# Performance work log

Measured on AMD Instinct MI355X. Metric: run time of the kernel, lower is better.

Reference implementation:

```python
import jax, jax.numpy as jnp
import numpy as np

B, N, D = 1024, 8192, 128
BETA = 0.25


def setup_inputs() -> dict:
    key = jax.random.key(0)
    kx, kw = jax.random.split(key)
    x = jax.random.normal(kx, (B, D), dtype=jnp.float32)
    # nn.Embedding weight init: uniform(-1/num_embeddings, 1/num_embeddings)
    W = jax.random.uniform(kw, (N, D), dtype=jnp.float32, minval=-1.0 / N, maxval=1.0 / N)
    return {"x": x, "W": W}


def reference(x, W):
    # Squared L2 distances: (B, N) via expansion; single GEMM for the cross term.
    dist = (x * x).sum(axis=1, keepdims=True) - 2.0 * (x @ W.T) + (W * W).sum(axis=1)[None, :]
    # (-dist).topk(k=1) == argmin(dist); torch keeps the k dim -> ind is (B, 1)
    ind = jnp.argmin(dist, axis=1)[:, None]
    q = W[ind]  # (B, 1, D) codebook gather (matches torch embedding(ind) shape)
    # Faithful to source: (B, D) broadcasts against (B, 1, D) -> (B, B, D)
    loss = BETA * jnp.mean((x - jax.lax.stop_gradient(q)) ** 2) + jnp.mean((jax.lax.stop_gradient(x) - q) ** 2)
    quantized = x + jax.lax.stop_gradient(q - x)  # straight-through; (B, B, D) per source broadcast
    return quantized, ind, loss
```

## Files before the change

kernel.cpp:

```cpp
#include <hip/hip_runtime.h>
#include <stdint.h>

typedef float vfloat4 __attribute__((ext_vector_type(4)));

static const long long QN       = 134217728LL;
static const long long IND_OFF  = QN;
static const long long LOSS_OFF = QN + 1024;
static const long long PVAL_OFF = 1022LL * 131072 + 128;
static const long long PIDX_OFF = 1023LL * 131072 + 128;

#define WS_W2  0
#define WS_X2  8192
#define WS_SX  9216
#define WS_SQ  9344
#define WS_SX2 9472
#define WS_SQ2 9473

__global__ void k_zero(float* __restrict__ ws) {
    int i = blockIdx.x * 256 + threadIdx.x;
    if (i < 258) ws[WS_SX + i] = 0.0f;
}

__global__ void k_rowsq(const float* __restrict__ P, float* __restrict__ o) {
    int n = blockIdx.x * 256 + threadIdx.x;
    const float4* pr = (const float4*)P + (size_t)n * 32;
    float s = 0.0f;
#pragma unroll 8
    for (int t = 0; t < 32; ++t) {
        float4 v = pr[t];
        s += v.x * v.x + v.y * v.y + v.z * v.z + v.w * v.w;
    }
    o[n] = s;
}

__global__ void k_colsums(const float* __restrict__ p, long long rowStride,
                          float* __restrict__ scol, float* __restrict__ s2out) {
    __shared__ float sh[256];
    const int tid = threadIdx.x;
    const int d = tid & 127, g = tid >> 7;
    const int r0 = blockIdx.x * 128;
    float sum = 0.0f, s2 = 0.0f;
    for (int r = r0 + g; r < r0 + 128; r += 2) {
        float v = p[(size_t)r * rowStride + d];
        sum += v;
        s2 += v * v;
    }
    sh[tid] = sum;
    __syncthreads();
    if (tid < 128) atomicAdd(&scol[d], sh[tid] + sh[tid + 128]);
    __syncthreads();
    sh[tid] = s2;
    __syncthreads();
    for (int s = 128; s > 0; s >>= 1) {
        if (tid < s) sh[tid] += sh[tid + s];
        __syncthreads();
    }
    if (tid == 0) atomicAdd(s2out, sh[0]);
}

__global__ __launch_bounds__(256) void k_score(
    const float* __restrict__ x, const float* __restrict__ W,
    const float* __restrict__ w2, const float* __restrict__ x2,
    float* __restrict__ pval, int* __restrict__ pidx) {
    __shared__ float Xs[32][132];
    __shared__ float Wst[32][132];
    const int tid = threadIdx.x;
    const int tx = tid & 15, ty = tid >> 4;
    const int n0 = blockIdx.x * 128, m0 = blockIdx.y * 128;
    const float4* xv = (const float4*)x;
    const float4* wv = (const float4*)W;

    float acc[8][8];
#pragma unroll
    for (int i = 0; i < 8; ++i)
#pragma unroll
        for (int j = 0; j < 8; ++j) acc[i][j] = 0.0f;

    for (int kc = 0; kc < 4; ++kc) {
#pragma unroll
        for (int it = 0; it < 4; ++it) {
            int f = it * 256 + tid;
            int m = f >> 3, kq = f & 7;
            float4 a = xv[(size_t)(m0 + m) * 32 + kc * 8 + kq];
            float4 b = wv[(size_t)(n0 + m) * 32 + kc * 8 + kq];
            Xs[kq * 4 + 0][m] = a.x;
            Xs[kq * 4 + 1][m] = a.y;
            Xs[kq * 4 + 2][m] = a.z;
            Xs[kq * 4 + 3][m] = a.w;
            Wst[kq * 4 + 0][m] = b.x;
            Wst[kq * 4 + 1][m] = b.y;
            Wst[kq * 4 + 2][m] = b.z;
            Wst[kq * 4 + 3][m] = b.w;
        }
        __syncthreads();
#pragma unroll 8
        for (int k = 0; k < 32; ++k) {
            float4 a0 = *(const float4*)&Xs[k][ty * 8];
            float4 a1 = *(const float4*)&Xs[k][ty * 8 + 4];
            float4 b0 = *(const float4*)&Wst[k][tx * 8];
            float4 b1 = *(const float4*)&Wst[k][tx * 8 + 4];
            float af[8] = {a0.x, a0.y, a0.z, a0.w, a1.x, a1.y, a1.z, a1.w};
            float bf[8] = {b0.x, b0.y, b0.z, b0.w, b1.x, b1.y, b1.z, b1.w};
#pragma unroll
            for (int i = 0; i < 8; ++i)
#pragma unroll
                for (int j = 0; j < 8; ++j) acc[i][j] += af[i] * bf[j];
        }
        __syncthreads();
    }

    float w2v[8];
#pragma unroll
    for (int j = 0; j < 8; ++j) w2v[j] = w2[n0 + tx * 8 + j];

#pragma unroll
    for (int i = 0; i < 8; ++i) {
        const int row = m0 + ty * 8 + i;
        const float xxv = x2[row];
        float bestv;
        int besti = n0 + tx * 8;
        {
            float t = xxv - 2.0f * acc[i][0];
            bestv = t + w2v[0];
        }
#pragma unroll
        for (int j = 1; j < 8; ++j) {
            float t = xxv - 2.0f * acc[i][j];
            float s = t + w2v[j];
            if (s < bestv) { bestv = s; besti = n0 + tx * 8 + j; }
        }
        for (int off = 1; off < 16; off <<= 1) {
            float ov = __shfl_xor(bestv, off, 64);
            int oi = __shfl_xor(besti, off, 64);
            if (ov < bestv || (ov == bestv && oi < besti)) { bestv = ov; besti = oi; }
        }
        if (tx == 0) {
            pval[row * 64 + blockIdx.x] = bestv;
            pidx[row * 64 + blockIdx.x] = besti;
        }
    }
}

__global__ void k_argmin(const float* __restrict__ W, const float* __restrict__ pval,
                         const int* __restrict__ pidx, float* __restrict__ out) {
    int r = blockIdx.x * 256 + threadIdx.x;
    float bestv = pval[r * 64];
    int besti = pidx[r * 64];
    for (int c = 1; c < 64; ++c) {
        float v = pval[r * 64 + c];
        if (v < bestv) { bestv = v; besti = pidx[r * 64 + c]; }
    }
    out[IND_OFF + r] = (float)besti;
    float4* q = (float4*)out + (size_t)r * 32768;
    const float4* wr = (const float4*)W + (size_t)besti * 32;
#pragma unroll 8
    for (int t = 0; t < 32; ++t) q[t] = wr[t];
}

__global__ void k_loss(const float* __restrict__ ws, float* __restrict__ out) {
    __shared__ float sh[128];
    int tid = threadIdx.x;
    sh[tid] = ws[WS_SX + tid] * ws[WS_SQ + tid];
    __syncthreads();
    for (int s = 64; s > 0; s >>= 1) {
        if (tid < s) sh[tid] += sh[tid + s];
        __syncthreads();
    }
    if (tid == 0) {
        double dot = (double)sh[0];
        double Sx2 = (double)ws[WS_SX2], Sq2 = (double)ws[WS_SQ2];
        double loss = 1.25 * (1024.0 * Sx2 + 1024.0 * Sq2 - 2.0 * dot) / 134217728.0;
        out[LOSS_OFF] = (float)loss;
    }
}

__global__ __launch_bounds__(256) void k_bcast(float* __restrict__ out) {
    const int i = blockIdx.x;
    const int t = threadIdx.x & 31;
    const int j0 = threadIdx.x >> 5;
    const vfloat4* src = (const vfloat4*)out + (size_t)i * 32768;
    vfloat4 q = src[t];
    vfloat4* dst = (vfloat4*)out + (size_t)i * 32768 + t;
    for (int j = j0; j < 1024; j += 8) {
        __builtin_nontemporal_store(q, dst + (size_t)j * 32);
    }
}

extern "C" void kernel_launch(void* const* d_in, const int* in_sizes, int n_in,
                              void* d_out, int out_size, void* d_ws, size_t ws_size,
                              hipStream_t stream) {
    const float* x = (const float*)d_in[0];
    const float* W = (const float*)d_in[1];
    float* out = (float*)d_out;
    float* ws = (float*)d_ws;

    hipLaunchKernelGGL(k_zero, dim3(2), dim3(256), 0, stream, ws);
    hipLaunchKernelGGL(k_rowsq, dim3(32), dim3(256), 0, stream, W, ws + WS_W2);
    hipLaunchKernelGGL(k_rowsq, dim3(4), dim3(256), 0, stream, x, ws + WS_X2);
    hipLaunchKernelGGL(k_colsums, dim3(8), dim3(256), 0, stream, x, (long long)128,
                       ws + WS_SX, ws + WS_SX2);
    hipLaunchKernelGGL(k_score, dim3(64, 8), dim3(256), 0, stream, x, W,
                       ws + WS_W2, ws + WS_X2, out + PVAL_OFF, (int*)(out + PIDX_OFF));
    hipLaunchKernelGGL(k_argmin, dim3(4), dim3(256), 0, stream, W, out + PVAL_OFF,
                       (const int*)(out + PIDX_OFF), out);
    hipLaunchKernelGGL(k_colsums, dim3(8), dim3(256), 0, stream, out, (long long)131072,
                       ws + WS_SQ, ws + WS_SQ2);
    hipLaunchKernelGGL(k_loss, dim3(1), dim3(128), 0, stream, ws, out);
    hipLaunchKernelGGL(k_bcast, dim3(1024), dim3(256), 0, stream, out);
}
```

Measured before the change: 640.9 us.

## Fuse prep, loss and broadcast kernels; split broadcast grid and drop nontemporal stores

Merges zeroing, row-norm and column-sum work into one prep kernel. The q column sums and the sum of q squared move into the argmin kernel through wave shuffles and atomics, and the loss reduction moves into block 0 of the broadcast kernel. Together this cuts the launch count from nine to four. The broadcast grid grows from 1024 to 4096 blocks, each writing a quarter of one slab, and the stores become ordinary rather than nontemporal, which may change write-back behaviour on the 512MB output. Loss is computed while other broadcast blocks are overwriting the output, but it reads only workspace, and the pval/pidx scratch that lives inside the output is consumed before the broadcast starts.

Result: no change. 635.9 us (-0.8%).

```diff
diff --git a/kernel.cpp b/kernel.cpp
--- a/kernel.cpp
+++ b/kernel.cpp
@@ -13,49 +13,39 @@
 #define WS_X2  8192
 #define WS_SX  9216
 #define WS_SQ  9344
-#define WS_SX2 9472
-#define WS_SQ2 9473
-
-__global__ void k_zero(float* __restrict__ ws) {
-    int i = blockIdx.x * 256 + threadIdx.x;
-    if (i < 258) ws[WS_SX + i] = 0.0f;
-}
-
-__global__ void k_rowsq(const float* __restrict__ P, float* __restrict__ o) {
-    int n = blockIdx.x * 256 + threadIdx.x;
-    const float4* pr = (const float4*)P + (size_t)n * 32;
-    float s = 0.0f;
+#define WS_SQ2 9472
+
+__global__ __launch_bounds__(256) void k_prep(const float* __restrict__ x,
+                                              const float* __restrict__ W,
+                                              float* __restrict__ ws) {
+    const int b = blockIdx.x, tid = threadIdx.x;
+    if (b < 36) {
+        const float4* pr = (b < 32) ? ((const float4*)W + (size_t)(b * 256 + tid) * 32)
+                                    : ((const float4*)x + (size_t)((b - 32) * 256 + tid) * 32);
+        float s = 0.0f;
 #pragma unroll 8
-    for (int t = 0; t < 32; ++t) {
-        float4 v = pr[t];
-        s += v.x * v.x + v.y * v.y + v.z * v.z + v.w * v.w;
-    }
-    o[n] = s;
-}
-
-__global__ void k_colsums(const float* __restrict__ p, long long rowStride,
-                          float* __restrict__ scol, float* __restrict__ s2out) {
-    __shared__ float sh[256];
-    const int tid = threadIdx.x;
-    const int d = tid & 127, g = tid >> 7;
-    const int r0 = blockIdx.x * 128;
-    float sum = 0.0f, s2 = 0.0f;
-    for (int r = r0 + g; r < r0 + 128; r += 2) {
-        float v = p[(size_t)r * rowStride + d];
-        sum += v;
-        s2 += v * v;
-    }
-    sh[tid] = sum;
-    __syncthreads();
-    if (tid < 128) atomicAdd(&scol[d], sh[tid] + sh[tid + 128]);
-    __syncthreads();
-    sh[tid] = s2;
-    __syncthreads();
-    for (int s = 128; s > 0; s >>= 1) {
-        if (tid < s) sh[tid] += sh[tid + s];
-        __syncthreads();
-    }
-    if (tid == 0) atomicAdd(s2out, sh[0]);
+        for (int t = 0; t < 32; ++t) {
+            float4 v = pr[t];
+            s += v.x * v.x + v.y * v.y + v.z * v.z + v.w * v.w;
+        }
+        if (b < 32) ws[WS_W2 + b * 256 + tid] = s;
+        else        ws[WS_X2 + (b - 32) * 256 + tid] = s;
+    } else {
+        __shared__ float sh[8][32];
+        const int c = tid & 31, g = tid >> 5;
+        const int col = (b - 36) * 32 + c;
+        float sum = 0.0f;
+        for (int r = g; r < 1024; r += 8) sum += x[(size_t)r * 128 + col];
+        sh[g][c] = sum;
+        __syncthreads();
+        if (g == 0) {
+            float t = 0.0f;
+#pragma unroll
+            for (int gg = 0; gg < 8; ++gg) t += sh[gg][c];
+            ws[WS_SX + col] = t;
+        }
+        if (b == 36 && tid < 129) ws[WS_SQ + tid] = 0.0f;
+    }
 }
 
 __global__ __launch_bounds__(256) void k_score(
@@ -141,9 +131,11 @@
     }
 }
 
-__global__ void k_argmin(const float* __restrict__ W, const float* __restrict__ pval,
-                         const int* __restrict__ pidx, float* __restrict__ out) {
-    int r = blockIdx.x * 256 + threadIdx.x;
+__global__ __launch_bounds__(256) void k_argmin(
+    const float* __restrict__ W, const float* __restrict__ w2,
+    const float* __restrict__ pval, const int* __restrict__ pidx,
+    float* __restrict__ out, float* __restrict__ ws) {
+    const int r = blockIdx.x * 256 + threadIdx.x;
     float bestv = pval[r * 64];
     int besti = pidx[r * 64];
     for (int c = 1; c < 64; ++c) {
@@ -151,38 +143,70 @@
         if (v < bestv) { bestv = v; besti = pidx[r * 64 + c]; }
     }
     out[IND_OFF + r] = (float)besti;
+
+    float q2 = w2[besti];
+    for (int off = 1; off < 64; off <<= 1) q2 += __shfl_xor(q2, off, 64);
+    if ((threadIdx.x & 63) == 0) atomicAdd(ws + WS_SQ2, q2);
+
     float4* q = (float4*)out + (size_t)r * 32768;
     const float4* wr = (const float4*)W + (size_t)besti * 32;
-#pragma unroll 8
-    for (int t = 0; t < 32; ++t) q[t] = wr[t];
-}
-
-__global__ void k_loss(const float* __restrict__ ws, float* __restrict__ out) {
-    __shared__ float sh[128];
-    int tid = threadIdx.x;
-    sh[tid] = ws[WS_SX + tid] * ws[WS_SQ + tid];
-    __syncthreads();
-    for (int s = 64; s > 0; s >>= 1) {
-        if (tid < s) sh[tid] += sh[tid + s];
-        __syncthreads();
-    }
-    if (tid == 0) {
-        double dot = (double)sh[0];
-        double Sx2 = (double)ws[WS_SX2], Sq2 = (double)ws[WS_SQ2];
-        double loss = 1.25 * (1024.0 * Sx2 + 1024.0 * Sq2 - 2.0 * dot) / 134217728.0;
-        out[LOSS_OFF] = (float)loss;
-    }
-}
-
-__global__ __launch_bounds__(256) void k_bcast(float* __restrict__ out) {
-    const int i = blockIdx.x;
-    const int t = threadIdx.x & 31;
-    const int j0 = threadIdx.x >> 5;
+    for (int t = 0; t < 32; ++t) {
+        float4 v = wr[t];
+        q[t] = v;
+        float4 s = v;
+        for (int off = 1; off < 64; off <<= 1) {
+            s.x += __shfl_xor(s.x, off, 64);
+            s.y += __shfl_xor(s.y, off, 64);
+            s.z += __shfl_xor(s.z, off, 64);
+            s.w += __shfl_xor(s.w, off, 64);
+        }
+        if ((threadIdx.x & 63) == 0) {
+            atomicAdd(ws + WS_SQ + t * 4 + 0, s.x);
+            atomicAdd(ws + WS_SQ + t * 4 + 1, s.y);
+            atomicAdd(ws + WS_SQ + t * 4 + 2, s.z);
+            atomicAdd(ws + WS_SQ + t * 4 + 3, s.w);
+        }
+    }
+}
+
+__global__ __launch_bounds__(256) void k_bcast(float* __restrict__ out,
+                                               const float* __restrict__ ws) {
+    const int bid = blockIdx.x, tid = threadIdx.x;
+    if (bid == 0) {
+        __shared__ float sh[256];
+        float dotv = (tid < 128) ? ws[WS_SX + tid] * ws[WS_SQ + tid] : 0.0f;
+        float sx2 = 0.0f;
+        for (int r = tid; r < 1024; r += 256) sx2 += ws[WS_X2 + r];
+        sh[tid] = dotv;
+        __syncthreads();
+        for (int s = 128; s > 0; s >>= 1) {
+            if (tid < s) sh[tid] += sh[tid + s];
+            __syncthreads();
+        }
+        const float dot = sh[0];
+        __syncthreads();
+        sh[tid] = sx2;
+        __syncthreads();
+        for (int s = 128; s > 0; s >>= 1) {
+            if (tid < s) sh[tid] += sh[tid + s];
+            __syncthreads();
+        }
+        if (tid == 0) {
+            double Sx2 = (double)sh[0], Sq2 = (double)ws[WS_SQ2];
+            double loss = 1.25 * (1024.0 * Sx2 + 1024.0 * Sq2 - 2.0 * (double)dot) / 134217728.0;
+            out[LOSS_OFF] = (float)loss;
+        }
+        __syncthreads();
+    }
+    const int i = bid >> 2;
+    const int quarter = bid & 3;
+    const int t = tid & 31;
+    const int jend = quarter * 256 + 256;
     const vfloat4* src = (const vfloat4*)out + (size_t)i * 32768;
-    vfloat4 q = src[t];
+    vfloat4 qv = src[t];
     vfloat4* dst = (vfloat4*)out + (size_t)i * 32768 + t;
-    for (int j = j0; j < 1024; j += 8) {
-        __builtin_nontemporal_store(q, dst + (size_t)j * 32);
+    for (int j = quarter * 256 + (tid >> 5); j < jend; j += 8) {
+        dst[(size_t)j * 32] = qv;
     }
 }
 
@@ -194,17 +218,10 @@
     float* out = (float*)d_out;
     float* ws = (float*)d_ws;
 
-    hipLaunchKernelGGL(k_zero, dim3(2), dim3(256), 0, stream, ws);
-    hipLaunchKernelGGL(k_rowsq, dim3(32), dim3(256), 0, stream, W, ws + WS_W2);
-    hipLaunchKernelGGL(k_rowsq, dim3(4), dim3(256), 0, stream, x, ws + WS_X2);
-    hipLaunchKernelGGL(k_colsums, dim3(8), dim3(256), 0, stream, x, (long long)128,
-                       ws + WS_SX, ws + WS_SX2);
+    hipLaunchKernelGGL(k_prep, dim3(40), dim3(256), 0, stream, x, W, ws);
     hipLaunchKernelGGL(k_score, dim3(64, 8), dim3(256), 0, stream, x, W,
                        ws + WS_W2, ws + WS_X2, out + PVAL_OFF, (int*)(out + PIDX_OFF));
-    hipLaunchKernelGGL(k_argmin, dim3(4), dim3(256), 0, stream, W, out + PVAL_OFF,
-                       (const int*)(out + PIDX_OFF), out);
-    hipLaunchKernelGGL(k_colsums, dim3(8), dim3(256), 0, stream, out, (long long)131072,
-                       ws + WS_SQ, ws + WS_SQ2);
-    hipLaunchKernelGGL(k_loss, dim3(1), dim3(128), 0, stream, ws, out);
-    hipLaunchKernelGGL(k_bcast, dim3(1024), dim3(256), 0, stream, out);
-}
+    hipLaunchKernelGGL(k_argmin, dim3(4), dim3(256), 0, stream, W, ws + WS_W2,
+                       out + PVAL_OFF, (const int*)(out + PIDX_OFF), out, ws);
+    hipLaunchKernelGGL(k_bcast, dim3(4096), dim3(256), 0, stream, out, ws);
+}
```
